# Kernel optimization log

Hardware: AMD Instinct MI355X
Metric: run time of the kernel (lower is better)

## Reference

```python
import jax, jax.numpy as jnp
import numpy as np

N, H = 8192, 256
TOP_K = 16          # k = min(top_k, N-1)
TEMPERATURE = 1.0
NEG_SLOPE = 0.2
NUM_SECTORS = 11


def setup_inputs() -> dict:
    key = jax.random.key(0)
    kE, kW, ka, ks, kA = jax.random.split(key, 5)
    embeddings = jax.random.normal(kE, (N, H), dtype=jnp.float32)
    # xavier-uniform-like scale for W (nn.Linear, bias=False)
    lim = float(np.sqrt(6.0 / (H + H)))
    W = jax.random.uniform(kW, (H, H), dtype=jnp.float32, minval=-lim, maxval=lim)
    # a ~ Normal(0, 1/sqrt(2H))
    a = jax.random.normal(ka, (2 * H,), dtype=jnp.float32) * (1.0 / np.sqrt(2 * H))
    sector_ids = jax.random.randint(ks, (N,), 0, NUM_SECTORS, dtype=jnp.int32)
    active_mask = jax.random.randint(kA, (N,), 0, 2, dtype=jnp.int32).astype(bool)
    return {"embeddings": embeddings, "W": W, "a": a,
            "sector_ids": sector_ids, "active_mask": active_mask}


def reference(embeddings, W, a, sector_ids, active_mask):
    # h = W(embeddings)  (torch Linear: x @ W.T)
    h = embeddings @ W.T                                   # [N, H]
    # attention[i,j] = leaky_relu(a . [h_i, h_j]) = leaky_relu(a1.h_i + a2.h_j)
    # (decomposition of the concat+matmul; same math, avoids O(N^2*2H) tensor)
    a1, a2 = a[:H], a[H:]
    s_i = h @ a1                                           # [N]
    s_j = h @ a2                                           # [N]
    att = jax.nn.leaky_relu(s_i[:, None] + s_j[None, :], NEG_SLOPE) / TEMPERATURE
    # combined mask: active pairs AND same sector
    mask = (active_mask[:, None] & active_mask[None, :]) \
           & (sector_ids[:, None] == sector_ids[None, :])  # [N, N]
    att = jnp.where(mask, att, -jnp.inf)
    k = min(TOP_K, N - 1)
    topk_values, topk_indices = jax.lax.top_k(att, k)      # [N, k] each
    valid = jnp.isfinite(topk_values)                      # invalid = masked-out slots
    # dense padded representation of (edge_index, edge_weight):
    # src = topk_indices, dst = row index, weight = topk_values where valid
    edge_weight = jnp.where(valid, topk_values, 0.0)
    return edge_weight, topk_indices, valid
```

## Files before the change

kernel.cpp:

```cpp
#include <hip/hip_runtime.h>

#define N 8192
#define H 256
#define TOPK 16
#define NSEC 11
#define NEG_SLOPE 0.2
#define NB 256
#define NT 256
#define RPB (N / NB)
#define NSL 8
#define SLICE (N / NSL)
#define IDX_SENT 0x7fffffff

__device__ __forceinline__ bool better(double av, int ai, double bv, int bi) {
    return (av > bv) || (av == bv && ai < bi);
}

__global__ __launch_bounds__(NT) void compute_v_s(
    const float* __restrict__ E, const float* __restrict__ W,
    const float* __restrict__ a,
    float* __restrict__ s1f, double* __restrict__ s2g)
{
    __shared__ float sa[2 * H];
    __shared__ double sv1[H];
    __shared__ double sv2[H];

    int t = threadIdx.x;
    int blk = blockIdx.x;
    int lane = t & 63;
    int w = t >> 6;

    sa[t] = a[t];
    sa[t + H] = a[t + H];
    __syncthreads();

    {
        double a1_0 = 0.0, a1_1 = 0.0, a1_2 = 0.0, a1_3 = 0.0;
        double a2_0 = 0.0, a2_1 = 0.0, a2_2 = 0.0, a2_3 = 0.0;
        for (int j = 0; j < H; j += 4) {
            double w0 = (double)W[(j + 0) * H + t];
            double w1 = (double)W[(j + 1) * H + t];
            double w2 = (double)W[(j + 2) * H + t];
            double w3 = (double)W[(j + 3) * H + t];
            a1_0 += w0 * (double)sa[j + 0];
            a1_1 += w1 * (double)sa[j + 1];
            a1_2 += w2 * (double)sa[j + 2];
            a1_3 += w3 * (double)sa[j + 3];
            a2_0 += w0 * (double)sa[H + j + 0];
            a2_1 += w1 * (double)sa[H + j + 1];
            a2_2 += w2 * (double)sa[H + j + 2];
            a2_3 += w3 * (double)sa[H + j + 3];
        }
        sv1[t] = (a1_0 + a1_1) + (a1_2 + a1_3);
        sv2[t] = (a2_0 + a2_1) + (a2_2 + a2_3);
    }
    __syncthreads();

    for (int q = 0; q < RPB / 4; ++q) {
        int r_loc = w + 4 * q;
        int row = blk * RPB + r_loc;
        const float4* Erow = (const float4*)(E + (size_t)row * H);
        float4 e = Erow[lane];
        int base = lane * 4;
        double acc1 = (double)e.x * sv1[base + 0] + (double)e.y * sv1[base + 1] +
                      (double)e.z * sv1[base + 2] + (double)e.w * sv1[base + 3];
        double acc2 = (double)e.x * sv2[base + 0] + (double)e.y * sv2[base + 1] +
                      (double)e.z * sv2[base + 2] + (double)e.w * sv2[base + 3];
        for (int o = 32; o > 0; o >>= 1) {
            acc1 += __shfl_down(acc1, o);
            acc2 += __shfl_down(acc2, o);
        }
        if (lane == 0) {
            s1f[row] = (float)acc1;
            s2g[row] = acc2;
        }
    }
}

__global__ __launch_bounds__(NT) void slice_topk(
    const double* __restrict__ s2g, const int* __restrict__ sec,
    const int* __restrict__ act,
    double* __restrict__ candV, int* __restrict__ candI,
    int* __restrict__ cnts)
{
    __shared__ double wV[4][TOPK];
    __shared__ int wI[4][TOPK];
    __shared__ int wCnt[4];

    int bx = blockIdx.x;
    int c = bx >> 3;
    int sl = bx & 7;
    int t = threadIdx.x;
    int lane = t & 63;
    int w = t >> 6;

    int j0 = sl * SLICE + 4 * t;
    int4 a4 = *(const int4*)(act + j0);
    int4 s4 = *(const int4*)(sec + j0);
    double2 d01 = *(const double2*)(s2g + j0);
    double2 d23 = *(const double2*)(s2g + j0 + 2);

    bool p0 = (a4.x != 0) && (s4.x == c);
    bool p1 = (a4.y != 0) && (s4.y == c);
    bool p2 = (a4.z != 0) && (s4.z == c);
    bool p3 = (a4.w != 0) && (s4.w == c);

    double v[4];
    int ix[4];
    v[0] = p0 ? d01.x : -INFINITY;  ix[0] = p0 ? (j0 + 0) : IDX_SENT;
    v[1] = p1 ? d01.y : -INFINITY;  ix[1] = p1 ? (j0 + 1) : IDX_SENT;
    v[2] = p2 ? d23.x : -INFINITY;  ix[2] = p2 ? (j0 + 2) : IDX_SENT;
    v[3] = p3 ? d23.y : -INFINITY;  ix[3] = p3 ? (j0 + 3) : IDX_SENT;

    int cnt = __popcll(__ballot(p0)) + __popcll(__ballot(p1)) +
              __popcll(__ballot(p2)) + __popcll(__ballot(p3));

    for (int r = 0; r < TOPK; ++r) {
        double bv = v[0];
        int bi = ix[0];
#pragma unroll
        for (int p = 1; p < 4; ++p)
            if (better(v[p], ix[p], bv, bi)) { bv = v[p]; bi = ix[p]; }
        for (int o = 32; o > 0; o >>= 1) {
            double ov = __shfl_xor(bv, o);
            int oi = __shfl_xor(bi, o);
            if (better(ov, oi, bv, bi)) { bv = ov; bi = oi; }
        }
#pragma unroll
        for (int p = 0; p < 4; ++p)
            if (ix[p] == bi) { v[p] = -INFINITY; ix[p] = IDX_SENT; }
        if (lane == 0) {
            wV[w][r] = bv;
            wI[w][r] = bi;
        }
    }
    if (lane == 0) wCnt[w] = cnt;
    __syncthreads();

    if (w == 0) {
        double mv = wV[lane >> 4][lane & 15];
        int mi = wI[lane >> 4][lane & 15];
        for (int r = 0; r < TOPK; ++r) {
            double bv = mv;
            int bi = mi;
            for (int o = 32; o > 0; o >>= 1) {
                double ov = __shfl_xor(bv, o);
                int oi = __shfl_xor(bi, o);
                if (better(ov, oi, bv, bi)) { bv = ov; bi = oi; }
            }
            if (mi == bi) { mv = -INFINITY; mi = IDX_SENT; }
            if (lane == 0) {
                candV[bx * TOPK + r] = bv;
                candI[bx * TOPK + r] = bi;
            }
        }
        if (lane == 0) cnts[bx] = wCnt[0] + wCnt[1] + wCnt[2] + wCnt[3];
    }
}

__global__ __launch_bounds__(64) void merge_topk(
    const double* __restrict__ candV, const int* __restrict__ candI,
    const int* __restrict__ cnts, const int* __restrict__ sec,
    const int* __restrict__ act,
    int* __restrict__ top_idx, int* __restrict__ fill_idx,
    int* __restrict__ m_arr)
{
    int c = blockIdx.x;
    int lane = threadIdx.x;

    const double* cbV = candV + (size_t)c * NSL * TOPK;
    const int* cbI = candI + (size_t)c * NSL * TOPK;
    double v0 = cbV[lane];
    int i0 = cbI[lane];
    double v1 = cbV[lane + 64];
    int i1 = cbI[lane + 64];

    for (int r = 0; r < TOPK; ++r) {
        double bv;
        int bi;
        if (better(v0, i0, v1, i1)) { bv = v0; bi = i0; }
        else                        { bv = v1; bi = i1; }
        for (int o = 32; o > 0; o >>= 1) {
            double ov = __shfl_xor(bv, o);
            int oi = __shfl_xor(bi, o);
            if (better(ov, oi, bv, bi)) { bv = ov; bi = oi; }
        }
        if (i0 == bi)      { v0 = -INFINITY; i0 = IDX_SENT; }
        else if (i1 == bi) { v1 = -INFINITY; i1 = IDX_SENT; }
        if (lane == 0) top_idx[c * TOPK + r] = (bi == IDX_SENT) ? -1 : bi;
    }

    int cl = (lane < NSL) ? cnts[c * NSL + lane] : 0;
    for (int o = 32; o > 0; o >>= 1) cl += __shfl_xor(cl, o);
    if (lane == 0) m_arr[c] = (cl < TOPK) ? cl : TOPK;

    int cnt2 = 0;
    for (int basej = 0; basej < N && cnt2 < TOPK; basej += 64) {
        int j = basej + lane;
        bool fail = !((act[j] != 0) && (sec[j] == c));
        unsigned long long mask = __ballot(fail);
        if (fail) {
            int rank = cnt2 + __popcll(mask & ((1ull << lane) - 1));
            if (rank < TOPK) fill_idx[c * TOPK + rank] = j;
        }
        cnt2 += __popcll(mask);
    }
}

__global__ __launch_bounds__(NT) void write_out(const float* __restrict__ s1f,
                                                const double* __restrict__ s2g,
                                                const int* __restrict__ sec,
                                                const int* __restrict__ act,
                                                const int* __restrict__ top_idx,
                                                const int* __restrict__ fill_idx,
                                                const int* __restrict__ m_arr,
                                                float* __restrict__ out) {
    int gid = blockIdx.x * NT + threadIdx.x;
    int i = gid >> 4;
    int slot = gid & 15;

    float wgt = 0.0f;
    float fidx;
    float fvalid = 0.0f;

    if (act[i] == 0) {
        fidx = (float)slot;
    } else {
        int c = sec[i];
        int m = m_arr[c];
        if (slot < m) {
            int j = top_idx[c * TOPK + slot];
            double x = (double)s1f[i] + s2g[j];
            double attv = (x >= 0.0) ? x : NEG_SLOPE * x;
            wgt = (float)attv;
            fvalid = 1.0f;
            fidx = (float)j;
        } else {
            fidx = (float)fill_idx[c * TOPK + (slot - m)];
        }
    }

    out[gid] = wgt;
    out[N * TOPK + gid] = fidx;
    out[2 * N * TOPK + gid] = fvalid;
}

extern "C" void kernel_launch(void* const* d_in, const int* in_sizes, int n_in,
                              void* d_out, int out_size, void* d_ws, size_t ws_size,
                              hipStream_t stream) {
    const float* E = (const float*)d_in[0];
    const float* W = (const float*)d_in[1];
    const float* a = (const float*)d_in[2];
    const int* sec = (const int*)d_in[3];
    const int* act = (const int*)d_in[4];

    char* ws = (char*)d_ws;
    double* s2g = (double*)ws;
    double* candV = s2g + N;
    float* s1f = (float*)(candV + NSEC * NSL * TOPK);
    int* candI = (int*)(s1f + N);
    int* cnts = candI + NSEC * NSL * TOPK;
    int* top_idx = cnts + NSEC * NSL;
    int* fill_idx = top_idx + NSEC * TOPK;
    int* m_arr = fill_idx + NSEC * TOPK;

    float* out = (float*)d_out;

    hipLaunchKernelGGL(compute_v_s, dim3(NB), dim3(NT), 0, stream,
                       E, W, a, s1f, s2g);
    hipLaunchKernelGGL(slice_topk, dim3(NSEC * NSL), dim3(NT), 0, stream,
                       s2g, sec, act, candV, candI, cnts);
    hipLaunchKernelGGL(merge_topk, dim3(NSEC), dim3(64), 0, stream,
                       candV, candI, cnts, sec, act, top_idx, fill_idx, m_arr);
    hipLaunchKernelGGL(write_out, dim3((N * TOPK) / NT), dim3(NT), 0, stream,
                       s1f, s2g, sec, act, top_idx, fill_idx, m_arr, out);
}
```

Measured before the change: 111.8 us.

## Fuse top-k merge into output kernel and split W reduction across 512 threads

```diff
diff --git a/kernel.cpp b/kernel.cpp
--- a/kernel.cpp
+++ b/kernel.cpp
@@ -16,12 +16,14 @@
     return (av > bv) || (av == bv && ai < bi);
 }
 
-__global__ __launch_bounds__(NT) void compute_v_s(
+__global__ __launch_bounds__(512) void compute_v_s(
     const float* __restrict__ E, const float* __restrict__ W,
     const float* __restrict__ a,
     float* __restrict__ s1f, double* __restrict__ s2g)
 {
     __shared__ float sa[2 * H];
+    __shared__ double part1[2][H];
+    __shared__ double part2[2][H];
     __shared__ double sv1[H];
     __shared__ double sv2[H];
 
@@ -31,17 +33,18 @@
     int w = t >> 6;
 
     sa[t] = a[t];
-    sa[t + H] = a[t + H];
     __syncthreads();
 
     {
+        int col = t & 255;
+        int g = t >> 8;
         double a1_0 = 0.0, a1_1 = 0.0, a1_2 = 0.0, a1_3 = 0.0;
         double a2_0 = 0.0, a2_1 = 0.0, a2_2 = 0.0, a2_3 = 0.0;
-        for (int j = 0; j < H; j += 4) {
-            double w0 = (double)W[(j + 0) * H + t];
-            double w1 = (double)W[(j + 1) * H + t];
-            double w2 = (double)W[(j + 2) * H + t];
-            double w3 = (double)W[(j + 3) * H + t];
+        for (int j = g * 128; j < g * 128 + 128; j += 4) {
+            double w0 = (double)W[(j + 0) * H + col];
+            double w1 = (double)W[(j + 1) * H + col];
+            double w2 = (double)W[(j + 2) * H + col];
+            double w3 = (double)W[(j + 3) * H + col];
             a1_0 += w0 * (double)sa[j + 0];
             a1_1 += w1 * (double)sa[j + 1];
             a1_2 += w2 * (double)sa[j + 2];
@@ -51,13 +54,18 @@
             a2_2 += w2 * (double)sa[H + j + 2];
             a2_3 += w3 * (double)sa[H + j + 3];
         }
-        sv1[t] = (a1_0 + a1_1) + (a1_2 + a1_3);
-        sv2[t] = (a2_0 + a2_1) + (a2_2 + a2_3);
-    }
-    __syncthreads();
-
-    for (int q = 0; q < RPB / 4; ++q) {
-        int r_loc = w + 4 * q;
+        part1[g][col] = (a1_0 + a1_1) + (a1_2 + a1_3);
+        part2[g][col] = (a2_0 + a2_1) + (a2_2 + a2_3);
+    }
+    __syncthreads();
+    if (t < H) {
+        sv1[t] = part1[0][t] + part1[1][t];
+        sv2[t] = part2[0][t] + part2[1][t];
+    }
+    __syncthreads();
+
+    for (int q = 0; q < RPB / 8; ++q) {
+        int r_loc = w + 8 * q;
         int row = blk * RPB + r_loc;
         const float4* Erow = (const float4*)(E + (size_t)row * H);
         float4 e = Erow[lane];
@@ -158,64 +166,63 @@
     }
 }
 
-__global__ __launch_bounds__(64) void merge_topk(
+__global__ __launch_bounds__(NT) void merge_write(
+    const float* __restrict__ s1f, const double* __restrict__ s2g,
+    const int* __restrict__ sec, const int* __restrict__ act,
     const double* __restrict__ candV, const int* __restrict__ candI,
-    const int* __restrict__ cnts, const int* __restrict__ sec,
-    const int* __restrict__ act,
-    int* __restrict__ top_idx, int* __restrict__ fill_idx,
-    int* __restrict__ m_arr)
+    const int* __restrict__ cnts,
+    float* __restrict__ out)
 {
-    int c = blockIdx.x;
-    int lane = threadIdx.x;
-
-    const double* cbV = candV + (size_t)c * NSL * TOPK;
-    const int* cbI = candI + (size_t)c * NSL * TOPK;
-    double v0 = cbV[lane];
-    int i0 = cbI[lane];
-    double v1 = cbV[lane + 64];
-    int i1 = cbI[lane + 64];
-
-    for (int r = 0; r < TOPK; ++r) {
-        double bv;
-        int bi;
-        if (better(v0, i0, v1, i1)) { bv = v0; bi = i0; }
-        else                        { bv = v1; bi = i1; }
-        for (int o = 32; o > 0; o >>= 1) {
-            double ov = __shfl_xor(bv, o);
-            int oi = __shfl_xor(bi, o);
-            if (better(ov, oi, bv, bi)) { bv = ov; bi = oi; }
-        }
-        if (i0 == bi)      { v0 = -INFINITY; i0 = IDX_SENT; }
-        else if (i1 == bi) { v1 = -INFINITY; i1 = IDX_SENT; }
-        if (lane == 0) top_idx[c * TOPK + r] = (bi == IDX_SENT) ? -1 : bi;
-    }
-
-    int cl = (lane < NSL) ? cnts[c * NSL + lane] : 0;
-    for (int o = 32; o > 0; o >>= 1) cl += __shfl_xor(cl, o);
-    if (lane == 0) m_arr[c] = (cl < TOPK) ? cl : TOPK;
-
-    int cnt2 = 0;
-    for (int basej = 0; basej < N && cnt2 < TOPK; basej += 64) {
-        int j = basej + lane;
-        bool fail = !((act[j] != 0) && (sec[j] == c));
-        unsigned long long mask = __ballot(fail);
-        if (fail) {
-            int rank = cnt2 + __popcll(mask & ((1ull << lane) - 1));
-            if (rank < TOPK) fill_idx[c * TOPK + rank] = j;
-        }
-        cnt2 += __popcll(mask);
-    }
-}
-
-__global__ __launch_bounds__(NT) void write_out(const float* __restrict__ s1f,
-                                                const double* __restrict__ s2g,
-                                                const int* __restrict__ sec,
-                                                const int* __restrict__ act,
-                                                const int* __restrict__ top_idx,
-                                                const int* __restrict__ fill_idx,
-                                                const int* __restrict__ m_arr,
-                                                float* __restrict__ out) {
-    int gid = blockIdx.x * NT + threadIdx.x;
+    __shared__ int sTop[NSEC][TOPK];
+    __shared__ int sFill[NSEC][TOPK];
+    __shared__ int sM[NSEC];
+
+    int t = threadIdx.x;
+    int lane = t & 63;
+    int w = t >> 6;
+
+    for (int c = w; c < NSEC; c += 4) {
+        const double* cbV = candV + (size_t)c * NSL * TOPK;
+        const int* cbI = candI + (size_t)c * NSL * TOPK;
+        double v0 = cbV[lane];
+        int i0 = cbI[lane];
+        double v1 = cbV[lane + 64];
+        int i1 = cbI[lane + 64];
+
+        for (int r = 0; r < TOPK; ++r) {
+            double bv;
+            int bi;
+            if (better(v0, i0, v1, i1)) { bv = v0; bi = i0; }
+            else                        { bv = v1; bi = i1; }
+            for (int o = 32; o > 0; o >>= 1) {
+                double ov = __shfl_xor(bv, o);
+                int oi = __shfl_xor(bi, o);
+                if (better(ov, oi, bv, bi)) { bv = ov; bi = oi; }
+            }
+            if (i0 == bi)      { v0 = -INFINITY; i0 = IDX_SENT; }
+            else if (i1 == bi) { v1 = -INFINITY; i1 = IDX_SENT; }
+            if (lane == 0) sTop[c][r] = (bi == IDX_SENT) ? -1 : bi;
+        }
+
+        int cl = (lane < NSL) ? cnts[c * NSL + lane] : 0;
+        for (int o = 32; o > 0; o >>= 1) cl += __shfl_xor(cl, o);
+        if (lane == 0) sM[c] = (cl < TOPK) ? cl : TOPK;
+
+        int cnt2 = 0;
+        for (int basej = 0; basej < N && cnt2 < TOPK; basej += 64) {
+            int j = basej + lane;
+            bool fail = !((act[j] != 0) && (sec[j] == c));
+            unsigned long long mask = __ballot(fail);
+            if (fail) {
+                int rank = cnt2 + __popcll(mask & ((1ull << lane) - 1));
+                if (rank < TOPK) sFill[c][rank] = j;
+            }
+            cnt2 += __popcll(mask);
+        }
+    }
+    __syncthreads();
+
+    int gid = blockIdx.x * NT + t;
     int i = gid >> 4;
     int slot = gid & 15;
 
@@ -227,16 +234,16 @@
         fidx = (float)slot;
     } else {
         int c = sec[i];
-        int m = m_arr[c];
+        int m = sM[c];
         if (slot < m) {
-            int j = top_idx[c * TOPK + slot];
+            int j = sTop[c][slot];
             double x = (double)s1f[i] + s2g[j];
             double attv = (x >= 0.0) ? x : NEG_SLOPE * x;
             wgt = (float)attv;
             fvalid = 1.0f;
             fidx = (float)j;
         } else {
-            fidx = (float)fill_idx[c * TOPK + (slot - m)];
+            fidx = (float)sFill[c][slot - m];
         }
     }
 
@@ -260,18 +267,12 @@
     float* s1f = (float*)(candV + NSEC * NSL * TOPK);
     int* candI = (int*)(s1f + N);
     int* cnts = candI + NSEC * NSL * TOPK;
-    int* top_idx = cnts + NSEC * NSL;
-    int* fill_idx = top_idx + NSEC * TOPK;
-    int* m_arr = fill_idx + NSEC * TOPK;
-
     float* out = (float*)d_out;
 
-    hipLaunchKernelGGL(compute_v_s, dim3(NB), dim3(NT), 0, stream,
+    hipLaunchKernelGGL(compute_v_s, dim3(NB), dim3(512), 0, stream,
                        E, W, a, s1f, s2g);
     hipLaunchKernelGGL(slice_topk, dim3(NSEC * NSL), dim3(NT), 0, stream,
                        s2g, sec, act, candV, candI, cnts);
-    hipLaunchKernelGGL(merge_topk, dim3(NSEC), dim3(64), 0, stream,
-                       candV, candI, cnts, sec, act, top_idx, fill_idx, m_arr);
-    hipLaunchKernelGGL(write_out, dim3((N * TOPK) / NT), dim3(NT), 0, stream,
-                       s1f, s2g, sec, act, top_idx, fill_idx, m_arr, out);
-}
+    hipLaunchKernelGGL(merge_write, dim3((N * TOPK) / NT), dim3(NT), 0, stream,
+                       s1f, s2g, sec, act, candV, candI, cnts, out);
+}
```

After: 127.3 us. 13.9% more time.
